# Performance work log

Measured on AMD Instinct MI355X. Metric: run time of the kernel, lower is better.

The kernel has to match this reference:

```python
import jax, jax.numpy as jnp
import numpy as np

N = 20000      # atom nodes
N_LG = 40000   # line-graph nodes (= undirected bonds)
E = 80000      # directed edges in original graph (= 2*N_LG)
E_LG = 200000  # line-graph edges
L = 5          # num_layer
D = 300        # emb_dim
NUM_ATOM, NUM_BOND, NUM_DIR, NUM_CHI = 120, 6, 3, 3
EPS = 1e-5


def setup_inputs() -> dict:
    key = jax.random.key(0)
    ks = jax.random.split(key, 24)
    ri = lambda k, shape, hi: jax.random.randint(k, shape, 0, hi, dtype=jnp.int32)
    nm = lambda k, shape: jax.random.normal(k, shape, dtype=jnp.float32) * 0.02
    inp = {}
    inp["x"] = ri(ks[0], (N, 2), 3)
    inp["edge_index"] = ri(ks[1], (2, E), N)
    inp["edge_attr"] = ri(ks[2], (E, 2), 3)
    inp["lg_x"] = ri(ks[3], (N_LG, 2), 3)
    inp["lg_edge_index"] = ri(ks[4], (2, E_LG), N_LG)
    inp["lg_edge_index_map"] = ri(ks[5], (2, N_LG), N)
    inp["lg_edge_index_map2"] = ri(ks[6], (E_LG,), N)
    # GNN-level embeddings
    inp["node_emb1"] = nm(ks[7], (NUM_ATOM, D))
    inp["node_emb2"] = nm(ks[8], (NUM_CHI, D))
    inp["gnn_edge_emb1"] = nm(ks[9], (NUM_BOND, D))
    inp["gnn_edge_emb2"] = nm(ks[10], (NUM_DIR, D))
    # per-layer main-graph GINConv params (stacked over layers)
    inp["g_emb1"] = nm(ks[11], (L, NUM_BOND, D))
    inp["g_emb2"] = nm(ks[12], (L, NUM_DIR, D))
    inp["g_w1"] = nm(ks[13], (L, D, 2 * D))
    inp["g_b1"] = jnp.zeros((L, 2 * D), jnp.float32)
    inp["g_w2"] = nm(ks[14], (L, 2 * D, D))
    inp["g_b2"] = jnp.zeros((L, D), jnp.float32)
    inp["g_gamma"] = jnp.ones((L, D), jnp.float32)
    inp["g_beta"] = jnp.zeros((L, D), jnp.float32)
    # per-layer line-graph GINConv params (is_lg=True -> atom/chirality tables)
    inp["lg_emb1"] = nm(ks[15], (L, NUM_ATOM, D))
    inp["lg_emb2"] = nm(ks[16], (L, NUM_CHI, D))
    inp["lg_w1"] = nm(ks[17], (L, D, 2 * D))
    inp["lg_b1"] = jnp.zeros((L, 2 * D), jnp.float32)
    inp["lg_w2"] = nm(ks[18], (L, 2 * D, D))
    inp["lg_b2"] = jnp.zeros((L, D), jnp.float32)
    inp["lg_gamma"] = jnp.ones((L, D), jnp.float32)
    inp["lg_beta"] = jnp.zeros((L, D), jnp.float32)
    return inp


def gin_conv(xn, src, dst, ea, emb1, emb2, sl_idx, w1, b1, w2, b2):
    # self loops appended at the end, with self_loop_attr = emb1[sl_idx] + emb2[0]
    n = xn.shape[0]
    sl = jnp.broadcast_to(emb1[sl_idx] + emb2[0], (n, xn.shape[1]))
    ea_full = jnp.concatenate([ea, sl], axis=0)
    idx = jnp.arange(n, dtype=src.dtype)
    src_f = jnp.concatenate([src, idx])
    dst_f = jnp.concatenate([dst, idx])
    msg = xn[src_f] + ea_full                      # gather + add
    aggr = jax.ops.segment_sum(msg, dst_f, num_segments=n)  # scatter-add
    return jnp.maximum(aggr @ w1 + b1, 0.0) @ w2 + b2        # MLP update


def batchnorm(h, g, b):
    # training-mode BN: batch mean / biased variance (matches torch normalization)
    mu = h.mean(0)
    var = h.var(0)
    return (h - mu) * jax.lax.rsqrt(var + EPS) * g + b


def reference(x, edge_index, edge_attr, lg_x, lg_edge_index, lg_edge_index_map,
              lg_edge_index_map2, node_emb1, node_emb2, gnn_edge_emb1, gnn_edge_emb2,
              g_emb1, g_emb2, g_w1, g_b1, g_w2, g_b2, g_gamma, g_beta,
              lg_emb1, lg_emb2, lg_w1, lg_b1, lg_w2, lg_b2, lg_gamma, lg_beta):
    h = node_emb1[x[:, 0]] + node_emb2[x[:, 1]]
    e = gnn_edge_emb1[lg_x[:, 0]] + gnn_edge_emb2[lg_x[:, 1]]
    h_list, e_list = [h], [e]
    lg_src, lg_dst = lg_edge_index[0], lg_edge_index[1]
    for layer in range(L):
        if layer == 0:
            ea = g_emb1[0][edge_attr[:, 0]] + g_emb2[0][edge_attr[:, 1]]
            src, dst = edge_index[0], edge_index[1]
        else:
            # edge_index rewritten from line-graph map; edge_attr = cat([e, e])
            ea = jnp.concatenate([e_list[layer], e_list[layer]], axis=0)
            src = jnp.concatenate([lg_edge_index_map[0], lg_edge_index_map[1]])
            dst = jnp.concatenate([lg_edge_index_map[1], lg_edge_index_map[0]])
        h = gin_conv(h_list[layer], src, dst, ea, g_emb1[layer], g_emb2[layer], 4,
                     g_w1[layer], g_b1[layer], g_w2[layer], g_b2[layer])
        h = batchnorm(h, g_gamma[layer], g_beta[layer])
        if layer < L - 1:
            h = jnp.maximum(h, 0.0)
        h_list.append(h)
        if layer == 0:
            xa = x[lg_edge_index_map2]  # int atom features of shared node
            lg_ea = lg_emb1[0][xa[:, 0]] + lg_emb2[0][xa[:, 1]]
        else:
            # lg_edge_attr = h[lg_edge_index_map2] from the PREVIOUS iteration's h
            lg_ea = h_list[layer][lg_edge_index_map2]
        e = gin_conv(e_list[layer], lg_src, lg_dst, lg_ea, lg_emb1[layer], lg_emb2[layer], 119,
                     lg_w1[layer], lg_b1[layer], lg_w2[layer], lg_b2[layer])
        e = batchnorm(e, lg_gamma[layer], lg_beta[layer])
        if layer < L - 1:
            e = jnp.maximum(e, 0.0)
        e_list.append(e)
    # (h_list, e_list) packed as one array: [L+1, N + N_LG, D]
    return jnp.concatenate([jnp.stack(h_list), jnp.stack(e_list)], axis=1)
```

## Files before the change

### kernel.cpp

```cpp
#include <hip/hip_runtime.h>

#define D 300

namespace {

constexpr int kN   = 20000;
constexpr int kNLG = 40000;
constexpr int kE   = 80000;
constexpr int kELG = 200000;
constexpr int kL   = 5;

constexpr int K1P = 320;
constexpr int N1P = 640;
constexpr int K2P = 640;
constexpr int N2P = 384;
constexpr int PQH = 320;
constexpr int MP_N   = 20096;
constexpr int MP_ALL = 60160;
constexpr int MAIN_TILES = 157;
constexpr int NRT = 470;
constexpr int NRP = 59;
constexpr int RH = 320;
constexpr int RQ = 40;
constexpr int NALL = kN + kNLG;

typedef __attribute__((ext_vector_type(8))) _Float16 half8;
typedef __attribute__((ext_vector_type(2))) _Float16 half2v;
typedef __attribute__((ext_vector_type(4))) float f32x4;

__device__ inline short f2h(float f) {
  _Float16 h = (_Float16)f;
  return __builtin_bit_cast(short, h);
}

__device__ inline float2 upk(unsigned u) {
  half2v h = __builtin_bit_cast(half2v, u);
  return make_float2((float)h.x, (float)h.y);
}

__device__ inline unsigned pk(float a, float b) {
  half2v h;
  h.x = (_Float16)a;
  h.y = (_Float16)b;
  return __builtin_bit_cast(unsigned, h);
}

__device__ inline void addrow(float* acc, uint4 r) {
  float2 t0 = upk(r.x), t1 = upk(r.y), t2 = upk(r.z), t3 = upk(r.w);
  acc[0] += t0.x; acc[1] += t0.y; acc[2] += t1.x; acc[3] += t1.y;
  acc[4] += t2.x; acc[5] += t2.y; acc[6] += t3.x; acc[7] += t3.y;
}

__device__ inline void unpk8(uint4 r, float* v) {
  float2 t0 = upk(r.x), t1 = upk(r.y), t2 = upk(r.z), t3 = upk(r.w);
  v[0] = t0.x; v[1] = t0.y; v[2] = t1.x; v[3] = t1.y;
  v[4] = t2.x; v[5] = t2.y; v[6] = t3.x; v[7] = t3.y;
}

__device__ inline uint4 pk4(const float* a) {
  uint4 r;
  r.x = pk(a[0], a[1]); r.y = pk(a[2], a[3]);
  r.z = pk(a[4], a[5]); r.w = pk(a[6], a[7]);
  return r;
}

__device__ inline void gload_lds16(const void* g, void* l) {
  __builtin_amdgcn_global_load_lds(
      (const __attribute__((address_space(1))) void*)g,
      (__attribute__((address_space(3))) void*)l, 16, 0, 0);
}


__global__ void k_init(float* __restrict__ stats, short* __restrict__ ab,
                       int* __restrict__ m0_cur, int* __restrict__ mL_cur,
                       int* __restrict__ lg_cur) {
  int g = blockIdx.x * blockDim.x + threadIdx.x;
  if (g < kL * 1200) stats[g] = 0.f;
  int np1 = (MP_N - kN) * K1P;
  int np2 = (MP_ALL - MP_N - kNLG) * K1P;
  if (g < np1) ab[(size_t)kN * K1P + g] = 0;
  if (g < np2) ab[(size_t)(MP_N + kNLG) * K1P + g] = 0;
  if (g < kN) { m0_cur[g] = 0; mL_cur[g] = 0; }
  if (g < kNLG) lg_cur[g] = 0;
}


__global__ void k_hist_all(const int* __restrict__ edge_index,
                           const int* __restrict__ lg_map,
                           const int* __restrict__ lg_ei,
                           const int* __restrict__ eattr,
                           const int* __restrict__ map2,
                           const int* __restrict__ x,
                           int* __restrict__ m0_cur, int* __restrict__ mL_cur,
                           int* __restrict__ lg_cur,
                           int* __restrict__ cam, int* __restrict__ cal) {
  int g = blockIdx.x * blockDim.x + threadIdx.x;
  if (g < kE) {
    atomicAdd(&m0_cur[edge_index[kE + g]], 1);
    cam[g] = eattr[2 * g] * 3 + eattr[2 * g + 1];
    return;
  }
  g -= kE;
  if (g < kNLG) { atomicAdd(&mL_cur[lg_map[kNLG + g]], 1); return; }
  g -= kNLG;
  if (g < kNLG) { atomicAdd(&mL_cur[lg_map[g]], 1); return; }
  g -= kNLG;
  if (g < kELG) {
    atomicAdd(&lg_cur[lg_ei[kELG + g]], 1);
    int a = map2[g];
    cal[g] = x[2 * a] * 3 + x[2 * a + 1];
  }
}

__device__ void scan_one(int* cursor, int* offs, int n) {
  __shared__ int part[256];
  int tid = threadIdx.x;
  int chunk = (n + 255) / 256;
  int s0 = tid * chunk;
  int s1 = min(n, s0 + chunk);
  int sum = 0;
  for (int i = s0; i < s1; ++i) sum += cursor[i];
  part[tid] = sum;
  __syncthreads();
  for (int off = 1; off < 256; off <<= 1) {
    int v = (tid >= off) ? part[tid - off] : 0;
    __syncthreads();
    part[tid] += v;
    __syncthreads();
  }
  int run = (tid == 0) ? 0 : part[tid - 1];
  for (int i = s0; i < s1; ++i) {
    int dv = cursor[i];
    offs[i] = run;
    cursor[i] = run;
    run += dv;
  }
  if (tid == 255) offs[n] = run;
}

__global__ __launch_bounds__(256) void k_scan3(
    int* __restrict__ m0_cur, int* __restrict__ m0_offs,
    int* __restrict__ mL_cur, int* __restrict__ mL_offs,
    int* __restrict__ lg_cur, int* __restrict__ lg_offs) {
  if (blockIdx.x == 0) scan_one(m0_cur, m0_offs, kN);
  else if (blockIdx.x == 1) scan_one(mL_cur, mL_offs, kN);
  else scan_one(lg_cur, lg_offs, kNLG);
}

__global__ void k_fill_all(const int* __restrict__ edge_index,
                           const int* __restrict__ lg_map,
                           const int* __restrict__ lg_ei,
                           int* __restrict__ m0_cur, int* __restrict__ m0_perm,
                           int* __restrict__ mL_cur, int* __restrict__ mL_perm,
                           int* __restrict__ lg_cur, int* __restrict__ lg_perm) {
  int g = blockIdx.x * blockDim.x + threadIdx.x;
  if (g < kE) {
    int pos = atomicAdd(&m0_cur[edge_index[kE + g]], 1);
    m0_perm[pos] = g;
    return;
  }
  g -= kE;
  if (g < kNLG) {
    int pos = atomicAdd(&mL_cur[lg_map[kNLG + g]], 1);
    mL_perm[pos] = g;
    return;
  }
  g -= kNLG;
  if (g < kNLG) {
    int pos = atomicAdd(&mL_cur[lg_map[g]], 1);
    mL_perm[pos] = kNLG + g;
    return;
  }
  g -= kNLG;
  if (g < kELG) {
    int pos = atomicAdd(&lg_cur[lg_ei[kELG + g]], 1);
    lg_perm[pos] = g;
  }
}


__device__ void cvt_w1(const float* W, short* Wt, int g) {
  int per = N1P * K1P;
  int l = g / per, rem = g - l * per;
  int n = rem / K1P, k = rem - n * K1P;
  float v = (n < 2 * D && k < D) ? W[(size_t)l * D * 2 * D + (size_t)k * 2 * D + n] : 0.f;
  Wt[g] = f2h(v);
}

__device__ void cvt_w2(const float* W, short* Wt, int g) {
  int per = N2P * K2P;
  int l = g / per, rem = g - l * per;
  int n = rem / K2P, k = rem - n * K2P;
  float v = (n < D && k < 2 * D) ? W[(size_t)l * 2 * D * D + (size_t)k * D + n] : 0.f;
  Wt[g] = f2h(v);
}

__global__ void k_precomp(const float* __restrict__ g1, const float* __restrict__ g2,
                          const float* __restrict__ l1, const float* __restrict__ l2,
                          const float* __restrict__ g_w1, const float* __restrict__ g_w2,
                          const float* __restrict__ lg_w1, const float* __restrict__ lg_w2,
                          float* __restrict__ slv, short* __restrict__ tcm,
                          short* __restrict__ tcl,
                          short* __restrict__ g_w1t, short* __restrict__ g_w2t,
                          short* __restrict__ lg_w1t, short* __restrict__ lg_w2t) {
  int g = blockIdx.x * blockDim.x + threadIdx.x;
  const int s1 = kL * N1P * K1P, s2 = kL * N2P * K2P;
  if (g < s1) { cvt_w1(g_w1, g_w1t, g); return; }
  g -= s1;
  if (g < s2) { cvt_w2(g_w2, g_w2t, g); return; }
  g -= s2;
  if (g < s1) { cvt_w1(lg_w1, lg_w1t, g); return; }
  g -= s1;
  if (g < s2) { cvt_w2(lg_w2, lg_w2t, g); return; }
  g -= s2;
  if (g < kL * 640) {
    int l = g / 640, rem = g - l * 640;
    int gr = rem / 320, c = rem - gr * 320;
    float v = 0.f;
    if (c < D) {
      if (gr == 0) v = g1[(size_t)l * 6 * D + 4 * D + c] + g2[(size_t)l * 3 * D + c];
      else         v = l1[(size_t)l * 120 * D + 119 * D + c] + l2[(size_t)l * 3 * D + c];
    }
    slv[g] = v;
    return;
  }
  g -= kL * 640;
  if (g < 18 * RH) {
    int p = g / RH, c = g - p * RH;
    float v = (c < D) ? g1[(size_t)(p / 3) * D + c] + g2[(size_t)(p % 3) * D + c] : 0.f;
    tcm[g] = f2h(v);
    return;
  }
  g -= 18 * RH;
  if (g < 360 * RH) {
    int p = g / RH, c = g - p * RH;
    float v = (c < D) ? l1[(size_t)(p / 3) * D + c] + l2[(size_t)(p % 3) * D + c] : 0.f;
    tcl[g] = f2h(v);
  }
}


__global__ void k_embed_all(const int* __restrict__ x, const int* __restrict__ lg_x,
                            const float* __restrict__ t1m, const float* __restrict__ t2m,
                            const float* __restrict__ t1l, const float* __restrict__ t2l,
                            float* __restrict__ outF, uint4* __restrict__ hist) {
  int g = blockIdx.x * blockDim.x + threadIdx.x;
  if (g >= NALL * RQ) return;
  int r = g / RQ, q = g - r * RQ;
  bool m = r < kN;
  int i = m ? r : r - kN;
  const int* ix = (m ? x : lg_x) + 2 * i;
  const float* t1 = (m ? t1m : t1l) + (size_t)ix[0] * D;
  const float* t2 = (m ? t2m : t2l) + (size_t)ix[1] * D;
  int c0 = q * 8;
  float y[8] = {0.f, 0.f, 0.f, 0.f, 0.f, 0.f, 0.f, 0.f};
  if (c0 < D) {
    float4 p0 = *(const float4*)(t1 + c0);
    float4 q0 = *(const float4*)(t2 + c0);
    y[0] = p0.x + q0.x; y[1] = p0.y + q0.y; y[2] = p0.z + q0.z; y[3] = p0.w + q0.w;
    *(float4*)(outF + (size_t)r * D + c0) = make_float4(y[0], y[1], y[2], y[3]);
    if (c0 + 8 <= D) {
      float4 p1 = *(const float4*)(t1 + c0 + 4);
      float4 q1 = *(const float4*)(t2 + c0 + 4);
      y[4] = p1.x + q1.x; y[5] = p1.y + q1.y; y[6] = p1.z + q1.z; y[7] = p1.w + q1.w;
      *(float4*)(outF + (size_t)r * D + c0 + 4) = make_float4(y[4], y[5], y[6], y[7]);
    }
  }
  hist[(size_t)r * RQ + q] = pk4(y);
}


__global__ __launch_bounds__(64) void k_gather_all0(
    const uint4* __restrict__ h16, const uint4* __restrict__ e16,
    const int* __restrict__ m_src, const int* __restrict__ lg_src,
    const int* __restrict__ cam, const int* __restrict__ cal,
    const uint4* __restrict__ tcm, const uint4* __restrict__ tcl,
    const float* __restrict__ slvM, const float* __restrict__ slvL,
    const int* __restrict__ m_offs, const int* __restrict__ m_perm,
    const int* __restrict__ l_offs, const int* __restrict__ l_perm,
    uint4* __restrict__ ab) {
  int node = blockIdx.x;
  int lane = threadIdx.x;
  bool act = lane < RQ;
  int ll = act ? lane : 0;
  bool isM = node < kN;
  int j = isM ? node : node - kN;
  const uint4* selfrow = isM ? (h16 + (size_t)node * RQ) : (e16 + (size_t)j * RQ);
  const float* sv = (isM ? slvM : slvL) + ll * 8;
  const int* offs = isM ? m_offs : l_offs;
  const int* permp = isM ? m_perm : l_perm;
  const uint4* bA = isM ? h16 : e16;
  const uint4* bB = isM ? tcm : tcl;
  const int* srcp = isM ? m_src : lg_src;
  const int* catp = isM ? cam : cal;

  float acc[8];
  {
    float vv[8];
    unpk8(selfrow[ll], vv);
#pragma unroll
    for (int i = 0; i < 8; ++i) acc[i] = vv[i] + sv[i];
  }

  int p0 = offs[j], p1 = offs[j + 1];
  for (int pb = p0; pb < p1; pb += 64) {
    int cnt = min(64, p1 - pb);
    int e_ = permp[pb + ((lane < cnt) ? lane : 0)];
    int ra = srcp[e_], rb = catp[e_];
    int t = 0;
    for (; t + 3 < cnt; t += 4) {
      int a0 = __shfl(ra, t),     b0 = __shfl(rb, t);
      int a1 = __shfl(ra, t + 1), b1 = __shfl(rb, t + 1);
      int a2 = __shfl(ra, t + 2), b2 = __shfl(rb, t + 2);
      int a3 = __shfl(ra, t + 3), b3 = __shfl(rb, t + 3);
      uint4 x0 = bA[(size_t)a0 * RQ + ll];
      uint4 y0 = bB[(size_t)b0 * RQ + ll];
      uint4 x1 = bA[(size_t)a1 * RQ + ll];
      uint4 y1 = bB[(size_t)b1 * RQ + ll];
      uint4 x2 = bA[(size_t)a2 * RQ + ll];
      uint4 y2 = bB[(size_t)b2 * RQ + ll];
      uint4 x3 = bA[(size_t)a3 * RQ + ll];
      uint4 y3 = bB[(size_t)b3 * RQ + ll];
      addrow(acc, x0); addrow(acc, y0);
      addrow(acc, x1); addrow(acc, y1);
      addrow(acc, x2); addrow(acc, y2);
      addrow(acc, x3); addrow(acc, y3);
    }
    for (; t < cnt; ++t) {
      int a0 = __shfl(ra, t), b0 = __shfl(rb, t);
      uint4 x0 = bA[(size_t)a0 * RQ + ll];
      uint4 y0 = bB[(size_t)b0 * RQ + ll];
      addrow(acc, x0); addrow(acc, y0);
    }
  }
  if (act) ab[(size_t)(isM ? node : MP_N + j) * RQ + ll] = pk4(acc);
}


__global__ __launch_bounds__(64) void k_gather_bnL(
    const uint4* __restrict__ pre, const float* __restrict__ coef,
    const int* __restrict__ lg_map, const int* __restrict__ lg_src,
    const int* __restrict__ map2,
    const float* __restrict__ slvM, const float* __restrict__ slvL,
    const int* __restrict__ m_offs, const int* __restrict__ m_perm,
    const int* __restrict__ l_offs, const int* __restrict__ l_perm,
    float* __restrict__ outF, uint4* __restrict__ ab) {
  int node = blockIdx.x;
  int lane = threadIdx.x;
  bool act = lane < RQ;
  int ll = act ? lane : 0;
  bool isM = node < kN;
  int j = isM ? node : node - kN;

  float aM[8], bM[8], aL[8], bL[8];
  {
    float4 t;
    t = *(const float4*)(coef + ll * 8);            aM[0]=t.x; aM[1]=t.y; aM[2]=t.z; aM[3]=t.w;
    t = *(const float4*)(coef + ll * 8 + 4);        aM[4]=t.x; aM[5]=t.y; aM[6]=t.z; aM[7]=t.w;
    t = *(const float4*)(coef + 320 + ll * 8);      bM[0]=t.x; bM[1]=t.y; bM[2]=t.z; bM[3]=t.w;
    t = *(const float4*)(coef + 320 + ll * 8 + 4);  bM[4]=t.x; bM[5]=t.y; bM[6]=t.z; bM[7]=t.w;
    t = *(const float4*)(coef + 640 + ll * 8);      aL[0]=t.x; aL[1]=t.y; aL[2]=t.z; aL[3]=t.w;
    t = *(const float4*)(coef + 640 + ll * 8 + 4);  aL[4]=t.x; aL[5]=t.y; aL[6]=t.z; aL[7]=t.w;
    t = *(const float4*)(coef + 960 + ll * 8);      bL[0]=t.x; bL[1]=t.y; bL[2]=t.z; bL[3]=t.w;
    t = *(const float4*)(coef + 960 + ll * 8 + 4);  bL[4]=t.x; bL[5]=t.y; bL[6]=t.z; bL[7]=t.w;
  }

  const float* sv = (isM ? slvM : slvL) + ll * 8;
  const int* offs = isM ? m_offs : l_offs;
  const int* permp = isM ? m_perm : l_perm;

  float acc[8];
  {
    int selfIdx = isM ? node : MP_N + j;
    float vv[8], y[8];
    unpk8(pre[(size_t)selfIdx * RQ + ll], vv);
#pragma unroll
    for (int i = 0; i < 8; ++i) {
      float a = isM ? aM[i] : aL[i];
      float b = isM ? bM[i] : bL[i];
      y[i] = fmaxf(a * vv[i] + b, 0.f);
      acc[i] = y[i] + sv[i];
    }
    if (act) {
      float* op = outF + (size_t)node * D + ll * 8;
      if (ll < 37) {
        *(float4*)op = make_float4(y[0], y[1], y[2], y[3]);
        *(float4*)(op + 4) = make_float4(y[4], y[5], y[6], y[7]);
      } else if (ll == 37) {
        *(float4*)op = make_float4(y[0], y[1], y[2], y[3]);
      }
    }
  }

  int p0 = offs[j], p1 = offs[j + 1];
  for (int pb = p0; pb < p1; pb += 64) {
    int cnt = min(64, p1 - pb);
    int e_ = permp[pb + ((lane < cnt) ? lane : 0)];
    int rh, re;
    if (isM) {
      rh = lg_map[e_];
      re = MP_N + ((e_ < kNLG) ? e_ : e_ - kNLG);
    } else {
      rh = map2[e_];
      re = MP_N + lg_src[e_];
    }
    int t = 0;
    for (; t + 1 < cnt; t += 2) {
      int h0 = __shfl(rh, t),     e0 = __shfl(re, t);
      int h1 = __shfl(rh, t + 1), e1 = __shfl(re, t + 1);
      uint4 xh0 = pre[(size_t)h0 * RQ + ll];
      uint4 xe0 = pre[(size_t)e0 * RQ + ll];
      uint4 xh1 = pre[(size_t)h1 * RQ + ll];
      uint4 xe1 = pre[(size_t)e1 * RQ + ll];
      float v[8];
      unpk8(xh0, v);
#pragma unroll
      for (int i = 0; i < 8; ++i) acc[i] += fmaxf(aM[i] * v[i] + bM[i], 0.f);
      unpk8(xe0, v);
#pragma unroll
      for (int i = 0; i < 8; ++i) acc[i] += fmaxf(aL[i] * v[i] + bL[i], 0.f);
      unpk8(xh1, v);
#pragma unroll
      for (int i = 0; i < 8; ++i) acc[i] += fmaxf(aM[i] * v[i] + bM[i], 0.f);
      unpk8(xe1, v);
#pragma unroll
      for (int i = 0; i < 8; ++i) acc[i] += fmaxf(aL[i] * v[i] + bL[i], 0.f);
    }
    if (t < cnt) {
      int h0 = __shfl(rh, t), e0 = __shfl(re, t);
      uint4 xh0 = pre[(size_t)h0 * RQ + ll];
      uint4 xe0 = pre[(size_t)e0 * RQ + ll];
      float v[8];
      unpk8(xh0, v);
#pragma unroll
      for (int i = 0; i < 8; ++i) acc[i] += fmaxf(aM[i] * v[i] + bM[i], 0.f);
      unpk8(xe0, v);
#pragma unroll
      for (int i = 0; i < 8; ++i) acc[i] += fmaxf(aL[i] * v[i] + bL[i], 0.f);
    }
  }
  if (act) ab[(size_t)(isM ? node : MP_N + j) * RQ + ll] = pk4(acc);
}


template<bool RELU, bool STATS>
__global__ __launch_bounds__(256) void k_mfma_gemm_dual(
    const short* __restrict__ A,
    const short* __restrict__ BtM, const short* __restrict__ BtL,
    const float* __restrict__ biasM, const float* __restrict__ biasL, int biasN,
    short* __restrict__ Cout, int Cstat, int Cwrite, int Cstride,
    int Astride, int Kloop, int NC,
    int mainLimit, int lgLimit,
    float* __restrict__ statsM, float* __restrict__ statsL) {
  __shared__ __align__(16) short ldsA[2][128 * 32];
  __shared__ __align__(16) short ldsB[2][128 * 32];
  __shared__ float sd[256];

  int bid = blockIdx.x;
  int xcd = bid & 7;
  int t0 = bid >> 3;
  int c = t0 % NC;
  int rr = t0 / NC;
  int rtile = rr * 8 + xcd;
  if (rtile >= NRT) return;

  const int tid = threadIdx.x;
  const int lane = tid & 63, w = tid >> 6;
  const bool isMain = rtile < MAIN_TILES;
  const short* Bt = isMain ? BtM : BtL;
  const float* bias = isMain ? biasM : biasL;
  const int rowLimit = isMain ? mainLimit : lgLimit;
  const int brow = rtile * 128;
  const int bcol = c * 128;
  const int wr = w >> 1, wc = w & 1;

  if (STATS) sd[tid] = 0.f;

  f32x4 acc[4][4] = {};

  const int sr = tid >> 2;
  const int sc = (tid & 3) * 8;

  auto stage = [&](int buf, int k0) {
    char* la = (char*)(&ldsA[buf][0]) + w * 1024;
    char* lb = (char*)(&ldsB[buf][0]) + w * 1024;
    const short* gA0 = A + (size_t)(brow + sr) * Astride + (k0 + sc);
    const short* gB0 = Bt + (size_t)(bcol + sr) * Astride + (k0 + sc);
    gload_lds16(gA0, la);
    gload_lds16(gA0 + (size_t)64 * Astride, la + 4096);
    gload_lds16(gB0, lb);
    gload_lds16(gB0 + (size_t)64 * Astride, lb + 4096);
  };

  const int nt = Kloop / 32;
  stage(0, 0);
  __syncthreads();

  for (int t = 0; t < nt; ++t) {
    int cb = t & 1;
    if (t + 1 < nt) stage(cb ^ 1, (t + 1) * 32);

    const int kq = (lane >> 4) * 16;
    const char* baseA = (const char*)(&ldsA[cb][0]);
    const char* baseB = (const char*)(&ldsB[cb][0]);
    half8 af[4], bf[4];
#pragma unroll
    for (int m = 0; m < 4; ++m) {
      int row = wr * 64 + m * 16 + (lane & 15);
      af[m] = *(const half8*)(baseA + row * 64 + kq);
    }
#pragma unroll
    for (int n = 0; n < 4; ++n) {
      int col = wc * 64 + n * 16 + (lane & 15);
      bf[n] = *(const half8*)(baseB + col * 64 + kq);
    }
#pragma unroll
    for (int m = 0; m < 4; ++m)
#pragma unroll
      for (int n = 0; n < 4; ++n)
        acc[m][n] = __builtin_amdgcn_mfma_f32_16x16x32_f16(af[m], bf[n], acc[m][n], 0, 0, 0);
    __syncthreads();
  }

  const int r0 = brow + wr * 64;
  const int c0 = bcol + wc * 64;
  float ps[4] = {}, pq[4] = {};
#pragma unroll
  for (int m = 0; m < 4; ++m) {
#pragma unroll
    for (int i = 0; i < 4; ++i) {
      int row = r0 + m * 16 + (lane >> 4) * 4 + i;
      bool rv = row < rowLimit;
#pragma unroll
      for (int n = 0; n < 4; ++n) {
        int col = c0 + n * 16 + (lane & 15);
        float bv = (col < biasN) ? bias[col] : 0.f;
        float v = acc[m][n][i] + bv;
        if (RELU) v = fmaxf(v, 0.f);
        if (rv && col < Cwrite) {
          Cout[(size_t)row * Cstride + col] = f2h(v);
          if (STATS && col < Cstat) { ps[n] += v; pq[n] += v * v; }
        }
      }
    }
  }

  if (STATS) {
#pragma unroll
    for (int n = 0; n < 4; ++n) {
      float s = ps[n], q = pq[n];
      s += __shfl_xor(s, 16); q += __shfl_xor(q, 16);
      s += __shfl_xor(s, 32); q += __shfl_xor(q, 32);
      if ((lane >> 4) == 0) {
        int cc = wc * 64 + n * 16 + (lane & 15);
        atomicAdd(&sd[cc], s);
        atomicAdd(&sd[128 + cc], q);
      }
    }
    __syncthreads();
    float* gs = isMain ? statsM : statsL;
    if (tid < 128) {
      int col = bcol + tid;
      if (col < Cstat) {
        atomicAdd(&gs[col], sd[tid]);
        atomicAdd(&gs[D + col], sd[128 + tid]);
      }
    }
  }
}


__global__ void k_bn_coef(const float* __restrict__ stats,
                          const float* __restrict__ gM, const float* __restrict__ bM,
                          const float* __restrict__ gL, const float* __restrict__ bL,
                          float* __restrict__ coef) {
  int t = blockIdx.x * blockDim.x + threadIdx.x;
  if (t >= 640) return;
  bool m = t < 320;
  int c = m ? t : t - 320;
  float a = 0.f, b = 0.f;
  if (c < D) {
    const float* s = stats + (m ? 0 : 600);
    float inv_n = m ? (1.f / kN) : (1.f / kNLG);
    float mu = s[c] * inv_n;
    float var = s[D + c] * inv_n - mu * mu;
    a = rsqrtf(var + 1e-5f) * (m ? gM : gL)[c];
    b = (m ? bM : bL)[c] - mu * a;
  }
  int base = m ? 0 : 640;
  coef[base + c] = a;
  coef[base + 320 + c] = b;
}


__global__ void k_bn_final(const uint4* __restrict__ pre, const float* __restrict__ coef,
                           float* __restrict__ outF) {
  int g = blockIdx.x * blockDim.x + threadIdx.x;
  if (g >= NALL * RQ) return;
  int r = g / RQ, q = g - r * RQ;
  bool m = r < kN;
  int pr = m ? r : MP_N + (r - kN);
  float v[8], y[8];
  unpk8(pre[(size_t)pr * RQ + q], v);
  const float* cb = coef + (m ? 0 : 640);
  float4 a0 = *(const float4*)(cb + q * 8);
  float4 a1 = *(const float4*)(cb + q * 8 + 4);
  float4 b0 = *(const float4*)(cb + 320 + q * 8);
  float4 b1 = *(const float4*)(cb + 320 + q * 8 + 4);
  y[0] = a0.x * v[0] + b0.x; y[1] = a0.y * v[1] + b0.y;
  y[2] = a0.z * v[2] + b0.z; y[3] = a0.w * v[3] + b0.w;
  y[4] = a1.x * v[4] + b1.x; y[5] = a1.y * v[5] + b1.y;
  y[6] = a1.z * v[6] + b1.z; y[7] = a1.w * v[7] + b1.w;
  float* op = outF + (size_t)r * D + q * 8;
  if (q < 37) {
    *(float4*)op = make_float4(y[0], y[1], y[2], y[3]);
    *(float4*)(op + 4) = make_float4(y[4], y[5], y[6], y[7]);
  } else if (q == 37) {
    *(float4*)op = make_float4(y[0], y[1], y[2], y[3]);
  }
}

}

extern "C" void kernel_launch(void* const* d_in, const int* in_sizes, int n_in,
                              void* d_out_v, int out_size, void* d_ws, size_t ws_size,
                              hipStream_t stream) {
  const int*   x            = (const int*)d_in[0];
  const int*   edge_index   = (const int*)d_in[1];
  const int*   edge_attr    = (const int*)d_in[2];
  const int*   lg_x         = (const int*)d_in[3];
  const int*   lg_edge_index= (const int*)d_in[4];
  const int*   lg_map       = (const int*)d_in[5];
  const int*   lg_map2      = (const int*)d_in[6];
  const float* node_emb1    = (const float*)d_in[7];
  const float* node_emb2    = (const float*)d_in[8];
  const float* gnn_e_emb1   = (const float*)d_in[9];
  const float* gnn_e_emb2   = (const float*)d_in[10];
  const float* g_emb1       = (const float*)d_in[11];
  const float* g_emb2       = (const float*)d_in[12];
  const float* g_w1         = (const float*)d_in[13];
  const float* g_b1         = (const float*)d_in[14];
  const float* g_w2         = (const float*)d_in[15];
  const float* g_b2         = (const float*)d_in[16];
  const float* g_gamma      = (const float*)d_in[17];
  const float* g_beta       = (const float*)d_in[18];
  const float* lg_emb1      = (const float*)d_in[19];
  const float* lg_emb2      = (const float*)d_in[20];
  const float* lg_w1        = (const float*)d_in[21];
  const float* lg_b1        = (const float*)d_in[22];
  const float* lg_w2        = (const float*)d_in[23];
  const float* lg_b2        = (const float*)d_in[24];
  const float* lg_gamma     = (const float*)d_in[25];
  const float* lg_beta      = (const float*)d_in[26];

  float* out = (float*)d_out_v;
  char*  ws  = (char*)d_ws;

  size_t off = 0;
  auto alloc = [&](size_t bytes) { void* p = ws + off; off = (off + bytes + 255) & ~(size_t)255; return p; };
  short* ab      = (short*)alloc((size_t)MP_ALL * K1P * 2);
  short* hidden  = (short*)alloc((size_t)MP_ALL * N1P * 2);
  short* pre2    = (short*)alloc((size_t)2 * MP_ALL * PQH * 2);
  short* hist    = (short*)alloc((size_t)NALL * RH * 2);
  short* g_w1t   = (short*)alloc((size_t)kL * N1P * K1P * 2);
  short* g_w2t   = (short*)alloc((size_t)kL * N2P * K2P * 2);
  short* lg_w1t  = (short*)alloc((size_t)kL * N1P * K1P * 2);
  short* lg_w2t  = (short*)alloc((size_t)kL * N2P * K2P * 2);
  float* stats   = (float*)alloc((kL * 1200 + 64) * 4);
  float* slv     = (float*)alloc(kL * 640 * 4);
  float* coef    = (float*)alloc(1280 * 4);
  short* tcm     = (short*)alloc(18 * RH * 2);
  short* tcl     = (short*)alloc(360 * RH * 2);
  int* cam     = (int*)alloc(kE * 4);
  int* cal     = (int*)alloc(kELG * 4);
  int* m0_offs = (int*)alloc((kN + 1) * 4);
  int* m0_cur  = (int*)alloc(kN * 4);
  int* m0_perm = (int*)alloc(kE * 4);
  int* mL_offs = (int*)alloc((kN + 1) * 4);
  int* mL_cur  = (int*)alloc(kN * 4);
  int* mL_perm = (int*)alloc(2 * kNLG * 4);
  int* lg_offs = (int*)alloc((kNLG + 1) * 4);
  int* lg_cur  = (int*)alloc(kNLG * 4);
  int* lg_perm = (int*)alloc(kELG * 4);

  auto hptr = [&](int l) { return out + (size_t)l * 60000 * D; };
  auto prep = [&](int s) { return pre2 + (size_t)s * MP_ALL * PQH; };

  dim3 b(256);

  k_init<<<(kNLG + 255) / 256, b, 0, stream>>>(stats, ab, m0_cur, mL_cur, lg_cur);
  {
    int tot = kE + 2 * kNLG + kELG;
    k_hist_all<<<(tot + 255) / 256, b, 0, stream>>>(edge_index, lg_map, lg_edge_index,
                                                    edge_attr, lg_map2, x,
                                                    m0_cur, mL_cur, lg_cur, cam, cal);
    k_scan3<<<3, b, 0, stream>>>(m0_cur, m0_offs, mL_cur, mL_offs, lg_cur, lg_offs);
    k_fill_all<<<(tot + 255) / 256, b, 0, stream>>>(edge_index, lg_map, lg_edge_index,
                                                    m0_cur, m0_perm, mL_cur, mL_perm,
                                                    lg_cur, lg_perm);
  }
  {
    int tot = 2 * kL * (N1P * K1P + N2P * K2P) + kL * 640 + 378 * RH;
    k_precomp<<<(tot + 255) / 256, b, 0, stream>>>(g_emb1, g_emb2, lg_emb1, lg_emb2,
                                                   g_w1, g_w2, lg_w1, lg_w2,
                                                   slv, tcm, tcl,
                                                   g_w1t, g_w2t, lg_w1t, lg_w2t);
  }
  k_embed_all<<<(NALL * RQ + 255) / 256, b, 0, stream>>>(x, lg_x, node_emb1, node_emb2,
                                                         gnn_e_emb1, gnn_e_emb2,
                                                         hptr(0), (uint4*)hist);

  int cur = 0;
  for (int l = 0; l < kL; ++l) {
    float* slot = stats + (size_t)l * 1200;
    const float* slvM = slv + (size_t)l * 640;
    const float* slvL = slvM + 320;

    if (l == 0)
      k_gather_all0<<<NALL, 64, 0, stream>>>(
          (const uint4*)hist, (const uint4*)(hist + (size_t)kN * RH),
          edge_index, lg_edge_index, cam, cal,
          (const uint4*)tcm, (const uint4*)tcl,
          slvM, slvL, m0_offs, m0_perm, lg_offs, lg_perm, (uint4*)ab);
    else
      k_gather_bnL<<<NALL, 64, 0, stream>>>(
          (const uint4*)prep(cur), coef, lg_map, lg_edge_index, lg_map2,
          slvM, slvL, mL_offs, mL_perm, lg_offs, lg_perm,
          hptr(l), (uint4*)ab);

    k_mfma_gemm_dual<true, false><<<8 * NRP * 5, b, 0, stream>>>(
        ab, g_w1t + (size_t)l * N1P * K1P, lg_w1t + (size_t)l * N1P * K1P,
        g_b1 + (size_t)l * 2 * D, lg_b1 + (size_t)l * 2 * D, 2 * D,
        hidden, 0, 608, N1P, K1P, K1P, 5, MP_ALL, MP_ALL, nullptr, nullptr);

    int nxt = cur ^ 1;
    k_mfma_gemm_dual<false, true><<<8 * NRP * 3, b, 0, stream>>>(
        hidden, g_w2t + (size_t)l * N2P * K2P, lg_w2t + (size_t)l * N2P * K2P,
        g_b2 + (size_t)l * D, lg_b2 + (size_t)l * D, D,
        prep(nxt), D, PQH, PQH, K2P, 608, 3, kN, MP_N + kNLG,
        slot, slot + 600);

    k_bn_coef<<<3, b, 0, stream>>>(slot,
                                   g_gamma + (size_t)l * D, g_beta + (size_t)l * D,
                                   lg_gamma + (size_t)l * D, lg_beta + (size_t)l * D, coef);
    cur = nxt;
  }

  k_bn_final<<<(NALL * RQ + 255) / 256, b, 0, stream>>>(
      (const uint4*)prep(cur), coef, hptr(kL));
}
```

Before: 1.344 ms.

## Precompute packed CSR edge records and fold BN coefficient kernel into consumers

The fill pass now writes packed int2 records (source row and attribute/target index) in CSR order, so the gather kernels read a single contiguous record per edge. This replaces the chain of perm lookup followed by scattered index loads. The separate per-layer batchnorm coefficient kernel is removed. Each gather and final BN thread now recomputes scale and shift from padded stats plus gamma/beta copied into a padded buffer by precomp. That cuts five small launches and their serialization, at the cost of redundant rsqrt work per block and extra index storage.

```diff
diff --git a/kernel.cpp b/kernel.cpp
--- a/kernel.cpp
+++ b/kernel.cpp
@@ -23,6 +23,7 @@
 constexpr int RH = 320;
 constexpr int RQ = 40;
 constexpr int NALL = kN + kNLG;
+constexpr int STL = 1280;
 
 typedef __attribute__((ext_vector_type(8))) _Float16 half8;
 typedef __attribute__((ext_vector_type(2))) _Float16 half2v;
@@ -70,12 +71,35 @@
       (__attribute__((address_space(3))) void*)l, 16, 0, 0);
 }
 
+__device__ inline void bn_coef8(const float* sb, const float* gb, int q,
+                                float inv_n, float* a, float* b) {
+  float4 s0 = *(const float4*)(sb + q * 8);
+  float4 s1 = *(const float4*)(sb + q * 8 + 4);
+  float4 q0 = *(const float4*)(sb + 320 + q * 8);
+  float4 q1 = *(const float4*)(sb + 320 + q * 8 + 4);
+  float4 g0 = *(const float4*)(gb + q * 8);
+  float4 g1 = *(const float4*)(gb + q * 8 + 4);
+  float4 e0 = *(const float4*)(gb + 320 + q * 8);
+  float4 e1 = *(const float4*)(gb + 320 + q * 8 + 4);
+  float su[8] = {s0.x, s0.y, s0.z, s0.w, s1.x, s1.y, s1.z, s1.w};
+  float sq[8] = {q0.x, q0.y, q0.z, q0.w, q1.x, q1.y, q1.z, q1.w};
+  float ga[8] = {g0.x, g0.y, g0.z, g0.w, g1.x, g1.y, g1.z, g1.w};
+  float be[8] = {e0.x, e0.y, e0.z, e0.w, e1.x, e1.y, e1.z, e1.w};
+#pragma unroll
+  for (int i = 0; i < 8; ++i) {
+    float mu = su[i] * inv_n;
+    float var = sq[i] * inv_n - mu * mu;
+    a[i] = rsqrtf(var + 1e-5f) * ga[i];
+    b[i] = be[i] - mu * a[i];
+  }
+}
+
 
 __global__ void k_init(float* __restrict__ stats, short* __restrict__ ab,
                        int* __restrict__ m0_cur, int* __restrict__ mL_cur,
                        int* __restrict__ lg_cur) {
   int g = blockIdx.x * blockDim.x + threadIdx.x;
-  if (g < kL * 1200) stats[g] = 0.f;
+  if (g < kL * STL) stats[g] = 0.f;
   int np1 = (MP_N - kN) * K1P;
   int np2 = (MP_ALL - MP_N - kNLG) * K1P;
   if (g < np1) ab[(size_t)kN * K1P + g] = 0;
@@ -88,28 +112,16 @@
 __global__ void k_hist_all(const int* __restrict__ edge_index,
                            const int* __restrict__ lg_map,
                            const int* __restrict__ lg_ei,
-                           const int* __restrict__ eattr,
-                           const int* __restrict__ map2,
-                           const int* __restrict__ x,
                            int* __restrict__ m0_cur, int* __restrict__ mL_cur,
-                           int* __restrict__ lg_cur,
-                           int* __restrict__ cam, int* __restrict__ cal) {
+                           int* __restrict__ lg_cur) {
   int g = blockIdx.x * blockDim.x + threadIdx.x;
-  if (g < kE) {
-    atomicAdd(&m0_cur[edge_index[kE + g]], 1);
-    cam[g] = eattr[2 * g] * 3 + eattr[2 * g + 1];
-    return;
-  }
+  if (g < kE) { atomicAdd(&m0_cur[edge_index[kE + g]], 1); return; }
   g -= kE;
   if (g < kNLG) { atomicAdd(&mL_cur[lg_map[kNLG + g]], 1); return; }
   g -= kNLG;
   if (g < kNLG) { atomicAdd(&mL_cur[lg_map[g]], 1); return; }
   g -= kNLG;
-  if (g < kELG) {
-    atomicAdd(&lg_cur[lg_ei[kELG + g]], 1);
-    int a = map2[g];
-    cal[g] = x[2 * a] * 3 + x[2 * a + 1];
-  }
+  if (g < kELG) atomicAdd(&lg_cur[lg_ei[kELG + g]], 1);
 }
 
 __device__ void scan_one(int* cursor, int* offs, int n) {
@@ -150,31 +162,37 @@
 __global__ void k_fill_all(const int* __restrict__ edge_index,
                            const int* __restrict__ lg_map,
                            const int* __restrict__ lg_ei,
-                           int* __restrict__ m0_cur, int* __restrict__ m0_perm,
-                           int* __restrict__ mL_cur, int* __restrict__ mL_perm,
-                           int* __restrict__ lg_cur, int* __restrict__ lg_perm) {
+                           const int* __restrict__ eattr,
+                           const int* __restrict__ map2,
+                           const int* __restrict__ x,
+                           int* __restrict__ m0_cur, int2* __restrict__ r0m,
+                           int* __restrict__ mL_cur, int2* __restrict__ rLm,
+                           int* __restrict__ lg_cur, int2* __restrict__ r0l,
+                           int2* __restrict__ rLl) {
   int g = blockIdx.x * blockDim.x + threadIdx.x;
   if (g < kE) {
     int pos = atomicAdd(&m0_cur[edge_index[kE + g]], 1);
-    m0_perm[pos] = g;
+    r0m[pos] = make_int2(edge_index[g], eattr[2 * g] * 3 + eattr[2 * g + 1]);
     return;
   }
   g -= kE;
   if (g < kNLG) {
     int pos = atomicAdd(&mL_cur[lg_map[kNLG + g]], 1);
-    mL_perm[pos] = g;
+    rLm[pos] = make_int2(lg_map[g], MP_N + g);
     return;
   }
   g -= kNLG;
   if (g < kNLG) {
     int pos = atomicAdd(&mL_cur[lg_map[g]], 1);
-    mL_perm[pos] = kNLG + g;
+    rLm[pos] = make_int2(lg_map[kNLG + g], MP_N + g);
     return;
   }
   g -= kNLG;
   if (g < kELG) {
     int pos = atomicAdd(&lg_cur[lg_ei[kELG + g]], 1);
-    lg_perm[pos] = g;
+    int a = map2[g];
+    r0l[pos] = make_int2(lg_ei[g], x[2 * a] * 3 + x[2 * a + 1]);
+    rLl[pos] = make_int2(a, MP_N + lg_ei[g]);
   }
 }
 
@@ -199,8 +217,10 @@
                           const float* __restrict__ l1, const float* __restrict__ l2,
                           const float* __restrict__ g_w1, const float* __restrict__ g_w2,
                           const float* __restrict__ lg_w1, const float* __restrict__ lg_w2,
+                          const float* __restrict__ g_gamma, const float* __restrict__ g_beta,
+                          const float* __restrict__ lg_gamma, const float* __restrict__ lg_beta,
                           float* __restrict__ slv, short* __restrict__ tcm,
-                          short* __restrict__ tcl,
+                          short* __restrict__ tcl, float* __restrict__ gbp,
                           short* __restrict__ g_w1t, short* __restrict__ g_w2t,
                           short* __restrict__ lg_w1t, short* __restrict__ lg_w2t) {
   int g = blockIdx.x * blockDim.x + threadIdx.x;
@@ -236,6 +256,19 @@
     int p = g / RH, c = g - p * RH;
     float v = (c < D) ? l1[(size_t)(p / 3) * D + c] + l2[(size_t)(p % 3) * D + c] : 0.f;
     tcl[g] = f2h(v);
+    return;
+  }
+  g -= 360 * RH;
+  if (g < kL * STL) {
+    int l = g / STL, rem = g - l * STL;
+    int seg = rem / 320, c = rem - seg * 320;
+    float v = 0.f;
+    if (c < D) {
+      const float* src = (seg == 0) ? g_gamma : (seg == 1) ? g_beta
+                       : (seg == 2) ? lg_gamma : lg_beta;
+      v = src[(size_t)l * D + c];
+    }
+    gbp[g] = v;
   }
 }
 
@@ -272,12 +305,10 @@
 
 __global__ __launch_bounds__(64) void k_gather_all0(
     const uint4* __restrict__ h16, const uint4* __restrict__ e16,
-    const int* __restrict__ m_src, const int* __restrict__ lg_src,
-    const int* __restrict__ cam, const int* __restrict__ cal,
+    const int2* __restrict__ r0m, const int2* __restrict__ r0l,
     const uint4* __restrict__ tcm, const uint4* __restrict__ tcl,
     const float* __restrict__ slvM, const float* __restrict__ slvL,
-    const int* __restrict__ m_offs, const int* __restrict__ m_perm,
-    const int* __restrict__ l_offs, const int* __restrict__ l_perm,
+    const int* __restrict__ m_offs, const int* __restrict__ l_offs,
     uint4* __restrict__ ab) {
   int node = blockIdx.x;
   int lane = threadIdx.x;
@@ -288,11 +319,9 @@
   const uint4* selfrow = isM ? (h16 + (size_t)node * RQ) : (e16 + (size_t)j * RQ);
   const float* sv = (isM ? slvM : slvL) + ll * 8;
   const int* offs = isM ? m_offs : l_offs;
-  const int* permp = isM ? m_perm : l_perm;
+  const int2* rows = isM ? r0m : r0l;
   const uint4* bA = isM ? h16 : e16;
   const uint4* bB = isM ? tcm : tcl;
-  const int* srcp = isM ? m_src : lg_src;
-  const int* catp = isM ? cam : cal;
 
   float acc[8];
   {
@@ -305,8 +334,8 @@
   int p0 = offs[j], p1 = offs[j + 1];
   for (int pb = p0; pb < p1; pb += 64) {
     int cnt = min(64, p1 - pb);
-    int e_ = permp[pb + ((lane < cnt) ? lane : 0)];
-    int ra = srcp[e_], rb = catp[e_];
+    int2 rr_ = rows[pb + ((lane < cnt) ? lane : 0)];
+    int ra = rr_.x, rb = rr_.y;
     int t = 0;
     for (; t + 3 < cnt; t += 4) {
       int a0 = __shfl(ra, t),     b0 = __shfl(rb, t);
@@ -338,12 +367,12 @@
 
 
 __global__ __launch_bounds__(64) void k_gather_bnL(
-    const uint4* __restrict__ pre, const float* __restrict__ coef,
-    const int* __restrict__ lg_map, const int* __restrict__ lg_src,
-    const int* __restrict__ map2,
+    const uint4* __restrict__ pre,
+    const float* __restrict__ stp,
+    const float* __restrict__ gbp,
+    const int2* __restrict__ rLm, const int2* __restrict__ rLl,
     const float* __restrict__ slvM, const float* __restrict__ slvL,
-    const int* __restrict__ m_offs, const int* __restrict__ m_perm,
-    const int* __restrict__ l_offs, const int* __restrict__ l_perm,
+    const int* __restrict__ m_offs, const int* __restrict__ l_offs,
     float* __restrict__ outF, uint4* __restrict__ ab) {
   int node = blockIdx.x;
   int lane = threadIdx.x;
@@ -353,21 +382,12 @@
   int j = isM ? node : node - kN;
 
   float aM[8], bM[8], aL[8], bL[8];
-  {
-    float4 t;
-    t = *(const float4*)(coef + ll * 8);            aM[0]=t.x; aM[1]=t.y; aM[2]=t.z; aM[3]=t.w;
-    t = *(const float4*)(coef + ll * 8 + 4);        aM[4]=t.x; aM[5]=t.y; aM[6]=t.z; aM[7]=t.w;
-    t = *(const float4*)(coef + 320 + ll * 8);      bM[0]=t.x; bM[1]=t.y; bM[2]=t.z; bM[3]=t.w;
-    t = *(const float4*)(coef + 320 + ll * 8 + 4);  bM[4]=t.x; bM[5]=t.y; bM[6]=t.z; bM[7]=t.w;
-    t = *(const float4*)(coef + 640 + ll * 8);      aL[0]=t.x; aL[1]=t.y; aL[2]=t.z; aL[3]=t.w;
-    t = *(const float4*)(coef + 640 + ll * 8 + 4);  aL[4]=t.x; aL[5]=t.y; aL[6]=t.z; aL[7]=t.w;
-    t = *(const float4*)(coef + 960 + ll * 8);      bL[0]=t.x; bL[1]=t.y; bL[2]=t.z; bL[3]=t.w;
-    t = *(const float4*)(coef + 960 + ll * 8 + 4);  bL[4]=t.x; bL[5]=t.y; bL[6]=t.z; bL[7]=t.w;
-  }
+  bn_coef8(stp, gbp, ll, 1.f / kN, aM, bM);
+  bn_coef8(stp + 640, gbp + 640, ll, 1.f / kNLG, aL, bL);
 
   const float* sv = (isM ? slvM : slvL) + ll * 8;
   const int* offs = isM ? m_offs : l_offs;
-  const int* permp = isM ? m_perm : l_perm;
+  const int2* rows = isM ? rLm : rLl;
 
   float acc[8];
   {
@@ -395,15 +415,8 @@
   int p0 = offs[j], p1 = offs[j + 1];
   for (int pb = p0; pb < p1; pb += 64) {
     int cnt = min(64, p1 - pb);
-    int e_ = permp[pb + ((lane < cnt) ? lane : 0)];
-    int rh, re;
-    if (isM) {
-      rh = lg_map[e_];
-      re = MP_N + ((e_ < kNLG) ? e_ : e_ - kNLG);
-    } else {
-      rh = map2[e_];
-      re = MP_N + lg_src[e_];
-    }
+    int2 rr_ = rows[pb + ((lane < cnt) ? lane : 0)];
+    int rh = rr_.x, re = rr_.y;
     int t = 0;
     for (; t + 1 < cnt; t += 2) {
       int h0 = __shfl(rh, t),     e0 = __shfl(re, t);
@@ -563,54 +576,28 @@
       int col = bcol + tid;
       if (col < Cstat) {
         atomicAdd(&gs[col], sd[tid]);
-        atomicAdd(&gs[D + col], sd[128 + tid]);
+        atomicAdd(&gs[320 + col], sd[128 + tid]);
       }
     }
   }
 }
 
 
-__global__ void k_bn_coef(const float* __restrict__ stats,
-                          const float* __restrict__ gM, const float* __restrict__ bM,
-                          const float* __restrict__ gL, const float* __restrict__ bL,
-                          float* __restrict__ coef) {
-  int t = blockIdx.x * blockDim.x + threadIdx.x;
-  if (t >= 640) return;
-  bool m = t < 320;
-  int c = m ? t : t - 320;
-  float a = 0.f, b = 0.f;
-  if (c < D) {
-    const float* s = stats + (m ? 0 : 600);
-    float inv_n = m ? (1.f / kN) : (1.f / kNLG);
-    float mu = s[c] * inv_n;
-    float var = s[D + c] * inv_n - mu * mu;
-    a = rsqrtf(var + 1e-5f) * (m ? gM : gL)[c];
-    b = (m ? bM : bL)[c] - mu * a;
-  }
-  int base = m ? 0 : 640;
-  coef[base + c] = a;
-  coef[base + 320 + c] = b;
-}
-
-
-__global__ void k_bn_final(const uint4* __restrict__ pre, const float* __restrict__ coef,
+__global__ void k_bn_final(const uint4* __restrict__ pre,
+                           const float* __restrict__ stp, const float* __restrict__ gbp,
                            float* __restrict__ outF) {
   int g = blockIdx.x * blockDim.x + threadIdx.x;
   if (g >= NALL * RQ) return;
   int r = g / RQ, q = g - r * RQ;
   bool m = r < kN;
   int pr = m ? r : MP_N + (r - kN);
+  float a[8], b[8];
+  bn_coef8(stp + (m ? 0 : 640), gbp + (m ? 0 : 640), q,
+           m ? (1.f / kN) : (1.f / kNLG), a, b);
   float v[8], y[8];
   unpk8(pre[(size_t)pr * RQ + q], v);
-  const float* cb = coef + (m ? 0 : 640);
-  float4 a0 = *(const float4*)(cb + q * 8);
-  float4 a1 = *(const float4*)(cb + q * 8 + 4);
-  float4 b0 = *(const float4*)(cb + 320 + q * 8);
-  float4 b1 = *(const float4*)(cb + 320 + q * 8 + 4);
-  y[0] = a0.x * v[0] + b0.x; y[1] = a0.y * v[1] + b0.y;
-  y[2] = a0.z * v[2] + b0.z; y[3] = a0.w * v[3] + b0.w;
-  y[4] = a1.x * v[4] + b1.x; y[5] = a1.y * v[5] + b1.y;
-  y[6] = a1.z * v[6] + b1.z; y[7] = a1.w * v[7] + b1.w;
+#pragma unroll
+  for (int i = 0; i < 8; ++i) y[i] = a[i] * v[i] + b[i];
   float* op = outF + (size_t)r * D + q * 8;
   if (q < 37) {
     *(float4*)op = make_float4(y[0], y[1], y[2], y[3]);
@@ -666,22 +653,21 @@
   short* g_w2t   = (short*)alloc((size_t)kL * N2P * K2P * 2);
   short* lg_w1t  = (short*)alloc((size_t)kL * N1P * K1P * 2);
   short* lg_w2t  = (short*)alloc((size_t)kL * N2P * K2P * 2);
-  float* stats   = (float*)alloc((kL * 1200 + 64) * 4);
+  float* stats   = (float*)alloc(kL * STL * 4);
+  float* gbp     = (float*)alloc(kL * STL * 4);
   float* slv     = (float*)alloc(kL * 640 * 4);
-  float* coef    = (float*)alloc(1280 * 4);
   short* tcm     = (short*)alloc(18 * RH * 2);
   short* tcl     = (short*)alloc(360 * RH * 2);
-  int* cam     = (int*)alloc(kE * 4);
-  int* cal     = (int*)alloc(kELG * 4);
+  int2* r0m    = (int2*)alloc((size_t)kE * 8);
+  int2* r0l    = (int2*)alloc((size_t)kELG * 8);
+  int2* rLm    = (int2*)alloc((size_t)2 * kNLG * 8);
+  int2* rLl    = (int2*)alloc((size_t)kELG * 8);
   int* m0_offs = (int*)alloc((kN + 1) * 4);
   int* m0_cur  = (int*)alloc(kN * 4);
-  int* m0_perm = (int*)alloc(kE * 4);
   int* mL_offs = (int*)alloc((kN + 1) * 4);
   int* mL_cur  = (int*)alloc(kN * 4);
-  int* mL_perm = (int*)alloc(2 * kNLG * 4);
   int* lg_offs = (int*)alloc((kNLG + 1) * 4);
   int* lg_cur  = (int*)alloc(kNLG * 4);
-  int* lg_perm = (int*)alloc(kELG * 4);
 
   auto hptr = [&](int l) { return out + (size_t)l * 60000 * D; };
   auto prep = [&](int s) { return pre2 + (size_t)s * MP_ALL * PQH; };
@@ -692,18 +678,19 @@
   {
     int tot = kE + 2 * kNLG + kELG;
     k_hist_all<<<(tot + 255) / 256, b, 0, stream>>>(edge_index, lg_map, lg_edge_index,
-                                                    edge_attr, lg_map2, x,
-                                                    m0_cur, mL_cur, lg_cur, cam, cal);
+                                                    m0_cur, mL_cur, lg_cur);
     k_scan3<<<3, b, 0, stream>>>(m0_cur, m0_offs, mL_cur, mL_offs, lg_cur, lg_offs);
     k_fill_all<<<(tot + 255) / 256, b, 0, stream>>>(edge_index, lg_map, lg_edge_index,
-                                                    m0_cur, m0_perm, mL_cur, mL_perm,
-                                                    lg_cur, lg_perm);
+                                                    edge_attr, lg_map2, x,
+                                                    m0_cur, r0m, mL_cur, rLm,
+                                                    lg_cur, r0l, rLl);
   }
   {
-    int tot = 2 * kL * (N1P * K1P + N2P * K2P) + kL * 640 + 378 * RH;
+    int tot = 2 * kL * (N1P * K1P + N2P * K2P) + kL * 640 + 378 * RH + kL * STL;
     k_precomp<<<(tot + 255) / 256, b, 0, stream>>>(g_emb1, g_emb2, lg_emb1, lg_emb2,
                                                    g_w1, g_w2, lg_w1, lg_w2,
-                                                   slv, tcm, tcl,
+                                                   g_gamma, g_beta, lg_gamma, lg_beta,
+                                                   slv, tcm, tcl, gbp,
                                                    g_w1t, g_w2t, lg_w1t, lg_w2t);
   }
   k_embed_all<<<(NALL * RQ + 255) / 256, b, 0, stream>>>(x, lg_x, node_emb1, node_emb2,
@@ -712,20 +699,20 @@
 
   int cur = 0;
   for (int l = 0; l < kL; ++l) {
-    float* slot = stats + (size_t)l * 1200;
+    float* slot = stats + (size_t)l * STL;
     const float* slvM = slv + (size_t)l * 640;
     const float* slvL = slvM + 320;
 
     if (l == 0)
       k_gather_all0<<<NALL, 64, 0, stream>>>(
           (const uint4*)hist, (const uint4*)(hist + (size_t)kN * RH),
-          edge_index, lg_edge_index, cam, cal,
-          (const uint4*)tcm, (const uint4*)tcl,
-          slvM, slvL, m0_offs, m0_perm, lg_offs, lg_perm, (uint4*)ab);
+          r0m, r0l, (const uint4*)tcm, (const uint4*)tcl,
+          slvM, slvL, m0_offs, lg_offs, (uint4*)ab);
     else
       k_gather_bnL<<<NALL, 64, 0, stream>>>(
-          (const uint4*)prep(cur), coef, lg_map, lg_edge_index, lg_map2,
-          slvM, slvL, mL_offs, mL_perm, lg_offs, lg_perm,
+          (const uint4*)prep(cur),
+          stats + (size_t)(l - 1) * STL, gbp + (size_t)(l - 1) * STL,
+          rLm, rLl, slvM, slvL, mL_offs, lg_offs,
           hptr(l), (uint4*)ab);
 
     k_mfma_gemm_dual<true, false><<<8 * NRP * 5, b, 0, stream>>>(
@@ -738,14 +725,11 @@
         hidden, g_w2t + (size_t)l * N2P * K2P, lg_w2t + (size_t)l * N2P * K2P,
         g_b2 + (size_t)l * D, lg_b2 + (size_t)l * D, D,
         prep(nxt), D, PQH, PQH, K2P, 608, 3, kN, MP_N + kNLG,
-        slot, slot + 600);
-
-    k_bn_coef<<<3, b, 0, stream>>>(slot,
-                                   g_gamma + (size_t)l * D, g_beta + (size_t)l * D,
-                                   lg_gamma + (size_t)l * D, lg_beta + (size_t)l * D, coef);
+        slot, slot + 640);
     cur = nxt;
   }
 
   k_bn_final<<<(NALL * RQ + 255) / 256, b, 0, stream>>>(
-      (const uint4*)prep(cur), coef, hptr(kL));
-}
+      (const uint4*)prep(cur),
+      stats + (size_t)(kL - 1) * STL, gbp + (size_t)(kL - 1) * STL, hptr(kL));
+}
```

New measurement: 1.321 ms. Within noise of the previous version (-1.7%).
